# Performance work log

Measured on AMD Instinct MI355X. Metric: run time of the kernel, lower is better.

The kernel has to match this reference:

```python
import jax, jax.numpy as jnp
import numpy as np

DEPTH = 6
N_LEAF = 2 ** DEPTH          # 64
GATE_COUNT = N_LEAF - 1      # 63
IN_F = 512
OUT_F = 512
BATCH = 1024


def setup_inputs() -> dict:
    key = jax.random.key(0)
    k1, k2, k3 = jax.random.split(key, 3)
    x = jax.random.normal(k1, (BATCH, IN_F), dtype=jnp.float32)
    gw = jax.random.normal(k2, (IN_F, GATE_COUNT), dtype=jnp.float32)
    gb = jnp.zeros((GATE_COUNT,), dtype=jnp.float32)
    pw = jax.random.normal(k3, (OUT_F, IN_F, N_LEAF), dtype=jnp.float32)
    pb = jnp.zeros((OUT_F, N_LEAF), dtype=jnp.float32)
    return {"x": x, "gw": gw, "gb": gb, "pw": pw, "pb": pb}


def _leaf_probs(x, gw, gb, depth):
    # gatings: sigmoid(x @ gw + gb), shape [B, gate_count]
    g = jax.nn.sigmoid(x @ gw + gb)
    B = x.shape[0]
    dens = jnp.ones((B, 1), dtype=x.dtype)  # root density
    offset = 0
    for d in range(depth):
        n = 2 ** d
        gp = g[:, offset:offset + n]                    # parent gatings [B, n]
        # left child multiplies by g, right child by (1 - g), interleaved
        pair = jnp.stack([gp, 1.0 - gp], axis=-1).reshape(B, 2 * n)
        dens = jnp.repeat(dens, 2, axis=1) * pair        # [B, 2n]
        offset += n
    return dens  # [B, n_leaf]


def reference(x, gw, gb, pw, pb):
    leaf = _leaf_probs(x, gw, gb, DEPTH)                 # [B, L]
    # per-leaf linear projections, then mix with leaf probabilities
    y = jnp.einsum('bi,oil->bol', x, pw)                 # [B, O, L]
    out = jnp.einsum('bol,bl->bo', y, leaf) + leaf @ pb.T
    return out
```

## Files before the change

kernel.cpp:

```cpp
#include <hip/hip_runtime.h>
#include <hip/hip_bf16.h>

#define TDEPTH 6
#define NLEAF 64
#define NGATE 63
#define INF 512
#define OUTF 512
#define BATCH 1024

#define BM 128
#define BN 32
#define SPLITK 16
#define THREADS 128
#define NPL 32

typedef __attribute__((ext_vector_type(4)))  float f32x4;
typedef __attribute__((ext_vector_type(16))) float f32x16;
typedef __attribute__((ext_vector_type(8)))  __bf16 bf16x8;

__device__ __forceinline__ bf16x8 pack8(f32x4 a, f32x4 b) {
  bf16x8 w;
  w[0] = (__bf16)a[0]; w[1] = (__bf16)a[1];
  w[2] = (__bf16)a[2]; w[3] = (__bf16)a[3];
  w[4] = (__bf16)b[0]; w[5] = (__bf16)b[1];
  w[6] = (__bf16)b[2]; w[7] = (__bf16)b[3];
  return w;
}

__global__ __launch_bounds__(256) void prep_kernel(
    const float* __restrict__ x, const float* __restrict__ gw,
    const float* __restrict__ gb, const float* __restrict__ pw,
    const float* __restrict__ pb, float* __restrict__ leaf,
    __bf16* __restrict__ pwb) {
  const int tid = threadIdx.x;
  if (blockIdx.x < 256) {
    const int wid = tid >> 6, lane = tid & 63;
    const int b = blockIdx.x * 4 + wid;
    __shared__ float g[4][NLEAF];
    if (lane < NGATE) {
      const float* xr = x + (size_t)b * INF;
      float a0 = 0.f, a1 = 0.f, a2 = 0.f, a3 = 0.f;
      #pragma unroll 4
      for (int i = 0; i < INF; i += 4) {
        a0 += xr[i + 0] * gw[(i + 0) * NGATE + lane];
        a1 += xr[i + 1] * gw[(i + 1) * NGATE + lane];
        a2 += xr[i + 2] * gw[(i + 2) * NGATE + lane];
        a3 += xr[i + 3] * gw[(i + 3) * NGATE + lane];
      }
      float t = (a0 + a1) + (a2 + a3) + gb[lane];
      g[wid][lane] = 1.0f / (1.0f + __expf(-t));
    }
    __syncthreads();
    float p = 1.0f;
    #pragma unroll
    for (int d = 0; d < TDEPTH; d++) {
      int prefix = lane >> (TDEPTH - 1 - d);
      int node = (1 << d) - 1 + (prefix >> 1);
      float gv = g[wid][node];
      p *= (prefix & 1) ? (1.0f - gv) : gv;
    }
    leaf[(size_t)b * NLEAF + lane] = p;
  } else {
    const unsigned Q = (blockIdx.x - 256) * 256 + tid;
    const unsigned tile = Q >> 8;
    const unsigned nb32 = tile / 513;
    const unsigned i = tile - nb32 * 513;
    const unsigned q = Q & 255;
    const unsigned r = q >> 3;
    const unsigned g = (q & 7) ^ (r & 7);
    const unsigned o = nb32 * 32 + r;
    const float* src = (i < INF) ? (pw + ((size_t)o * INF + i) * NLEAF + g * 8)
                                 : (pb + (size_t)o * NLEAF + g * 8);
    f32x4 a = *(const f32x4*)src, b = *(const f32x4*)(src + 4);
    *(bf16x8*)((char*)pwb + (size_t)Q * 16) = pack8(a, b);
  }
}

__device__ __forceinline__ void gload_lds16(const void* g, void* l) {
  __builtin_amdgcn_global_load_lds(
      (const __attribute__((address_space(1))) void*)g,
      (__attribute__((address_space(3))) void*)l, 16, 0, 0);
}

__global__ __launch_bounds__(THREADS, 4) void gemm_kernel(
    const __bf16* __restrict__ pwb, const float* __restrict__ x,
    const float* __restrict__ leaf, float* __restrict__ partial) {
  __shared__ __align__(16) __bf16 Bsm[3][2048];
  __shared__ __align__(16) __bf16 xsm[NPL][BM];

  const int tid = threadIdx.x, lane = tid & 63, w = tid >> 6;
  const int lo = lane & 31, half = lane >> 5;

  const int L = ((int)blockIdx.x & 7) * 256 + ((int)blockIdx.x >> 3);
  const int mb = L & 7;
  const int rest = L >> 3;
  const int nb = rest & 15, s = rest >> 4;
  const int m0 = mb * BM, o0 = nb * BN;
  const int cs = s * NPL;
  const int count = NPL + (s == SPLITK - 1 ? 1 : 0);

  bf16x8 lfb[2][4];
  #pragma unroll
  for (int mt = 0; mt < 2; mt++) {
    const float* lr =
        leaf + (size_t)(m0 + w * 64 + mt * 32 + lo) * NLEAF + half * 8;
    #pragma unroll
    for (int t4 = 0; t4 < 4; t4++)
      lfb[mt][t4] = pack8(*(const f32x4*)(lr + t4 * 16),
                          *(const f32x4*)(lr + t4 * 16 + 4));
  }

  {
    const float* src = x + (size_t)(m0 + tid) * INF + cs;
    #pragma unroll
    for (int c4 = 0; c4 < NPL / 4; c4++) {
      f32x4 v = *(const f32x4*)(src + c4 * 4);
      #pragma unroll
      for (int j = 0; j < 4; j++) xsm[c4 * 4 + j][tid] = (__bf16)v[j];
    }
  }

  const char* tb = (const char*)pwb + ((size_t)(nb * 513 + cs) << 12);

  auto stage = [&](char* dstb, int t) {
    const char* srcb = tb + ((size_t)t << 12);
    #pragma unroll
    for (int rnd = 0; rnd < 2; rnd++)
      gload_lds16(srcb + rnd * 2048 + tid * 16, dstb + rnd * 2048 + w * 1024);
  };

  f32x16 acc0 = (f32x16)(0.f), acc1 = (f32x16)(0.f);
  const unsigned swz = (unsigned)(lo & 7) << 4;

  auto do_step = [&](const char* bufc, int t) {
    float xv0 = 1.0f, xv1 = 1.0f;
    if (t < NPL) {
      xv0 = (float)xsm[t][w * 64 + lo];
      xv1 = (float)xsm[t][w * 64 + 32 + lo];
    }
    bf16x8 af[4];
    #pragma unroll
    for (int t4 = 0; t4 < 4; t4++)
      af[t4] = *(const bf16x8*)(bufc + lo * 128 +
                                (((unsigned)(t4 * 32 + half * 16)) ^ swz));
    {
      f32x16 D = (f32x16)(0.f);
      #pragma unroll
      for (int t4 = 0; t4 < 4; t4++)
        D = __builtin_amdgcn_mfma_f32_32x32x16_bf16(af[t4], lfb[0][t4], D, 0, 0, 0);
      acc0 += D * xv0;
    }
    {
      f32x16 D = (f32x16)(0.f);
      #pragma unroll
      for (int t4 = 0; t4 < 4; t4++)
        D = __builtin_amdgcn_mfma_f32_32x32x16_bf16(af[t4], lfb[1][t4], D, 0, 0, 0);
      acc1 += D * xv1;
    }
  };

  char* bA = (char*)&Bsm[0][0];
  char* bB = (char*)&Bsm[1][0];
  char* bC = (char*)&Bsm[2][0];

  stage(bA, 0);
  stage(bB, 1);
  __builtin_amdgcn_sched_barrier(0);
  asm volatile("s_waitcnt vmcnt(2) lgkmcnt(0)" ::: "memory");
  __builtin_amdgcn_s_barrier();
  __builtin_amdgcn_sched_barrier(0);

  for (int t = 0; t < count - 2; ++t) {
    stage(bC, t + 2);
    do_step(bA, t);
    __builtin_amdgcn_sched_barrier(0);
    asm volatile("s_waitcnt vmcnt(2) lgkmcnt(0)" ::: "memory");
    __builtin_amdgcn_s_barrier();
    __builtin_amdgcn_sched_barrier(0);
    char* tmp = bA; bA = bB; bB = bC; bC = tmp;
  }
  do_step(bA, count - 2);
  __builtin_amdgcn_sched_barrier(0);
  asm volatile("s_waitcnt vmcnt(0) lgkmcnt(0)" ::: "memory");
  __builtin_amdgcn_s_barrier();
  __builtin_amdgcn_sched_barrier(0);
  do_step(bB, count - 1);

  #pragma unroll
  for (int mt = 0; mt < 2; mt++) {
    float* dstb = partial + ((size_t)s * OUTF + o0) * BATCH +
                  (m0 + w * 64 + mt * 32);
    const f32x16 a = mt ? acc1 : acc0;
    #pragma unroll
    for (int e = 0; e < 16; e++) {
      int row = (e & 3) + 8 * (e >> 2) + 4 * half;
      dstb[(size_t)row * BATCH + lo] = a[e];
    }
  }
}

__global__ __launch_bounds__(256) void reduce_kernel(
    const float* __restrict__ partial, float* __restrict__ out) {
  __shared__ float tile[32][65];
  const int t = threadIdx.x;
  const int O0 = ((int)blockIdx.x >> 4) * 32;
  const int B0 = ((int)blockIdx.x & 15) * 64;
  #pragma unroll
  for (int rep = 0; rep < 8; rep++) {
    const int idx = rep * 256 + t;
    const int o = idx >> 6, b = idx & 63;
    float sum = 0.f;
    #pragma unroll
    for (int s = 0; s < SPLITK; s++)
      sum += partial[((size_t)s * OUTF + O0 + o) * BATCH + B0 + b];
    tile[o][b] = sum;
  }
  __syncthreads();
  #pragma unroll
  for (int rep = 0; rep < 8; rep++) {
    const int idx = rep * 256 + t;
    const int b = idx >> 5, o = idx & 31;
    out[(size_t)(B0 + b) * OUTF + O0 + o] = tile[o][b];
  }
}

extern "C" void kernel_launch(void* const* d_in, const int* in_sizes, int n_in,
                              void* d_out, int out_size, void* d_ws, size_t ws_size,
                              hipStream_t stream) {
  const float* x  = (const float*)d_in[0];
  const float* gw = (const float*)d_in[1];
  const float* gb = (const float*)d_in[2];
  const float* pw = (const float*)d_in[3];
  const float* pb = (const float*)d_in[4];
  float* out = (float*)d_out;

  float*  leaf    = (float*)d_ws;
  __bf16* pwb     = (__bf16*)((char*)d_ws + (256 << 10));
  float*  partial = (float*)((char*)d_ws + (256 << 10) + (size_t)16 * 513 * 4096);

  prep_kernel<<<256 + 8208, 256, 0, stream>>>(x, gw, gb, pw, pb, leaf, pwb);
  gemm_kernel<<<8 * 16 * SPLITK, THREADS, 0, stream>>>(pwb, x, leaf, partial);
  reduce_kernel<<<256, 256, 0, stream>>>(partial, out);
}
```

Before: 75.68 us.

## Retile gemm to single-wave blocks with fp16 and scaled-operand MFMA chaining

Moves the GEMM from bf16 to fp16. It switches to 64-thread single-wavefront blocks that each handle 64 batch rows by 32 output features over a split-K of 8. The x scaling is folded into the leaf operand with packed half multiplies, so the MFMAs accumulate directly instead of using a temporary plus a vector FMA. The block barriers go away because each wave now owns its LDS buffers, and the prep kernel's weight layout and swizzle change to match. The block's B-tile is larger, and folding x into the fp16 leaf values in half precision costs some accuracy and risks overflow or precision loss.

```diff
diff --git a/kernel.cpp b/kernel.cpp
--- a/kernel.cpp
+++ b/kernel.cpp
@@ -7,23 +7,19 @@
 #define INF 512
 #define OUTF 512
 #define BATCH 1024
-
-#define BM 128
-#define BN 32
-#define SPLITK 16
-#define THREADS 128
-#define NPL 32
-
+#define SPLITK 8
+#define NPL 64
+
+typedef _Float16 f16;
+typedef __attribute__((ext_vector_type(2)))  f16 f16x2;
+typedef __attribute__((ext_vector_type(8)))  f16 f16x8;
 typedef __attribute__((ext_vector_type(4)))  float f32x4;
 typedef __attribute__((ext_vector_type(16))) float f32x16;
-typedef __attribute__((ext_vector_type(8)))  __bf16 bf16x8;
-
-__device__ __forceinline__ bf16x8 pack8(f32x4 a, f32x4 b) {
-  bf16x8 w;
-  w[0] = (__bf16)a[0]; w[1] = (__bf16)a[1];
-  w[2] = (__bf16)a[2]; w[3] = (__bf16)a[3];
-  w[4] = (__bf16)b[0]; w[5] = (__bf16)b[1];
-  w[6] = (__bf16)b[2]; w[7] = (__bf16)b[3];
+
+__device__ __forceinline__ f16x8 pack8h(f32x4 a, f32x4 b) {
+  f16x8 w;
+  w[0] = (f16)a[0]; w[1] = (f16)a[1]; w[2] = (f16)a[2]; w[3] = (f16)a[3];
+  w[4] = (f16)b[0]; w[5] = (f16)b[1]; w[6] = (f16)b[2]; w[7] = (f16)b[3];
   return w;
 }
 
@@ -31,7 +27,7 @@
     const float* __restrict__ x, const float* __restrict__ gw,
     const float* __restrict__ gb, const float* __restrict__ pw,
     const float* __restrict__ pb, float* __restrict__ leaf,
-    __bf16* __restrict__ pwb) {
+    f16* __restrict__ pwh) {
   const int tid = threadIdx.x;
   if (blockIdx.x < 256) {
     const int wid = tid >> 6, lane = tid & 63;
@@ -60,20 +56,21 @@
       p *= (prefix & 1) ? (1.0f - gv) : gv;
     }
     leaf[(size_t)b * NLEAF + lane] = p;
-  } else {
-    const unsigned Q = (blockIdx.x - 256) * 256 + tid;
-    const unsigned tile = Q >> 8;
-    const unsigned nb32 = tile / 513;
-    const unsigned i = tile - nb32 * 513;
-    const unsigned q = Q & 255;
-    const unsigned r = q >> 3;
-    const unsigned g = (q & 7) ^ (r & 7);
-    const unsigned o = nb32 * 32 + r;
-    const float* src = (i < INF) ? (pw + ((size_t)o * INF + i) * NLEAF + g * 8)
-                                 : (pb + (size_t)o * NLEAF + g * 8);
-    f32x4 a = *(const f32x4*)src, b = *(const f32x4*)(src + 4);
-    *(bf16x8*)((char*)pwb + (size_t)Q * 16) = pack8(a, b);
-  }
+    return;
+  }
+  const unsigned Q = (blockIdx.x - 256) * 256 + tid;
+  const unsigned tile = Q >> 8;
+  const unsigned ot = tile / 513;
+  const unsigned i = tile - ot * 513;
+  const unsigned q = Q & 255;
+  const unsigned r = q >> 4, p = q & 15;
+  const unsigned v = p ^ r;
+  const unsigned o = ot * 32 + r + 16 * (v >> 3);
+  const unsigned kg = v & 7;
+  const float* src = (i < INF) ? (pw + ((size_t)o * INF + i) * NLEAF + kg * 8)
+                               : (pb + (size_t)o * NLEAF + kg * 8);
+  f32x4 a = *(const f32x4*)src, b = *(const f32x4*)(src + 4);
+  *(f16x8*)((char*)pwh + (size_t)Q * 16) = pack8h(a, b);
 }
 
 __device__ __forceinline__ void gload_lds16(const void* g, void* l) {
@@ -82,80 +79,82 @@
       (__attribute__((address_space(3))) void*)l, 16, 0, 0);
 }
 
-__global__ __launch_bounds__(THREADS, 4) void gemm_kernel(
-    const __bf16* __restrict__ pwb, const float* __restrict__ x,
+__global__ __launch_bounds__(64, 2) void gemm_kernel(
+    const f16* __restrict__ pwh, const float* __restrict__ x,
     const float* __restrict__ leaf, float* __restrict__ partial) {
-  __shared__ __align__(16) __bf16 Bsm[3][2048];
-  __shared__ __align__(16) __bf16 xsm[NPL][BM];
-
-  const int tid = threadIdx.x, lane = tid & 63, w = tid >> 6;
+  __shared__ __align__(16) char Bsm[3][4096];
+  __shared__ unsigned short xsm[NPL][64];
+
+  const int lane = threadIdx.x;
   const int lo = lane & 31, half = lane >> 5;
 
   const int L = ((int)blockIdx.x & 7) * 256 + ((int)blockIdx.x >> 3);
-  const int mb = L & 7;
-  const int rest = L >> 3;
-  const int nb = rest & 15, s = rest >> 4;
-  const int m0 = mb * BM, o0 = nb * BN;
+  const int bt = L & 15;
+  const int p = L >> 4;
+  const int ot = p & 15, s = p >> 4;
+  const int b0 = bt * 64;
   const int cs = s * NPL;
   const int count = NPL + (s == SPLITK - 1 ? 1 : 0);
 
-  bf16x8 lfb[2][4];
+  {
+    const float* xr = x + (size_t)(b0 + lane) * INF + cs;
+    #pragma unroll
+    for (int c4 = 0; c4 < NPL / 4; c4++) {
+      f32x4 v = *(const f32x4*)(xr + c4 * 4);
+      #pragma unroll
+      for (int j = 0; j < 4; j++)
+        xsm[c4 * 4 + j][lane] = __builtin_bit_cast(unsigned short, (f16)v[j]);
+    }
+  }
+
+  f16x8 lfb[2][4];
   #pragma unroll
   for (int mt = 0; mt < 2; mt++) {
-    const float* lr =
-        leaf + (size_t)(m0 + w * 64 + mt * 32 + lo) * NLEAF + half * 8;
+    const float* lr = leaf + (size_t)(b0 + mt * 32 + lo) * NLEAF + half * 8;
     #pragma unroll
     for (int t4 = 0; t4 < 4; t4++)
-      lfb[mt][t4] = pack8(*(const f32x4*)(lr + t4 * 16),
-                          *(const f32x4*)(lr + t4 * 16 + 4));
-  }
-
+      lfb[mt][t4] = pack8h(*(const f32x4*)(lr + t4 * 16),
+                           *(const f32x4*)(lr + t4 * 16 + 4));
+  }
+
+  unsigned rdoff[4];
   {
-    const float* src = x + (size_t)(m0 + tid) * INF + cs;
-    #pragma unroll
-    for (int c4 = 0; c4 < NPL / 4; c4++) {
-      f32x4 v = *(const f32x4*)(src + c4 * 4);
-      #pragma unroll
-      for (int j = 0; j < 4; j++) xsm[c4 * 4 + j][tid] = (__bf16)v[j];
-    }
-  }
-
-  const char* tb = (const char*)pwb + ((size_t)(nb * 513 + cs) << 12);
-
+    const unsigned r = (unsigned)(lo & 15);
+    const unsigned hb = ((unsigned)(lo >> 4)) * 128 + (unsigned)half * 16;
+    #pragma unroll
+    for (int t4 = 0; t4 < 4; t4++)
+      rdoff[t4] = r * 256 + ((hb + t4 * 32) ^ (r << 4));
+  }
+
+  const char* tb = (const char*)pwh + ((size_t)(ot * 513 + cs) << 12) +
+                   (size_t)lane * 16;
   auto stage = [&](char* dstb, int t) {
     const char* srcb = tb + ((size_t)t << 12);
     #pragma unroll
-    for (int rnd = 0; rnd < 2; rnd++)
-      gload_lds16(srcb + rnd * 2048 + tid * 16, dstb + rnd * 2048 + w * 1024);
+    for (int j = 0; j < 4; j++)
+      gload_lds16(srcb + j * 1024, dstb + j * 1024);
   };
 
   f32x16 acc0 = (f32x16)(0.f), acc1 = (f32x16)(0.f);
-  const unsigned swz = (unsigned)(lo & 7) << 4;
 
   auto do_step = [&](const char* bufc, int t) {
-    float xv0 = 1.0f, xv1 = 1.0f;
+    unsigned pr0 = 0x3C003C00u, pr1 = 0x3C003C00u;
     if (t < NPL) {
-      xv0 = (float)xsm[t][w * 64 + lo];
-      xv1 = (float)xsm[t][w * 64 + 32 + lo];
-    }
-    bf16x8 af[4];
-    #pragma unroll
-    for (int t4 = 0; t4 < 4; t4++)
-      af[t4] = *(const bf16x8*)(bufc + lo * 128 +
-                                (((unsigned)(t4 * 32 + half * 16)) ^ swz));
-    {
-      f32x16 D = (f32x16)(0.f);
-      #pragma unroll
-      for (int t4 = 0; t4 < 4; t4++)
-        D = __builtin_amdgcn_mfma_f32_32x32x16_bf16(af[t4], lfb[0][t4], D, 0, 0, 0);
-      acc0 += D * xv0;
-    }
-    {
-      f32x16 D = (f32x16)(0.f);
-      #pragma unroll
-      for (int t4 = 0; t4 < 4; t4++)
-        D = __builtin_amdgcn_mfma_f32_32x32x16_bf16(af[t4], lfb[1][t4], D, 0, 0, 0);
-      acc1 += D * xv1;
+      unsigned x0 = xsm[t][lo], x1 = xsm[t][32 + lo];
+      pr0 = x0 | (x0 << 16);
+      pr1 = x1 | (x1 << 16);
+    }
+    f16x2 v0 = __builtin_bit_cast(f16x2, pr0);
+    f16x2 v1 = __builtin_bit_cast(f16x2, pr1);
+    f16x8 xv80 = __builtin_shufflevector(v0, v0, 0, 1, 0, 1, 0, 1, 0, 1);
+    f16x8 xv81 = __builtin_shufflevector(v1, v1, 0, 1, 0, 1, 0, 1, 0, 1);
+    #pragma unroll
+    for (int t4 = 0; t4 < 4; t4++) {
+      f16x8 af = *(const f16x8*)(bufc + rdoff[t4]);
+      f16x8 s0 = lfb[0][t4] * xv80;
+      f16x8 s1 = lfb[1][t4] * xv81;
+      acc0 = __builtin_amdgcn_mfma_f32_32x32x16_f16(af, s0, acc0, 0, 0, 0);
+      acc1 = __builtin_amdgcn_mfma_f32_32x32x16_f16(af, s1, acc1, 0, 0, 0);
     }
   };
 
@@ -165,37 +164,25 @@
 
   stage(bA, 0);
   stage(bB, 1);
-  __builtin_amdgcn_sched_barrier(0);
-  asm volatile("s_waitcnt vmcnt(2) lgkmcnt(0)" ::: "memory");
-  __builtin_amdgcn_s_barrier();
-  __builtin_amdgcn_sched_barrier(0);
+  asm volatile("s_waitcnt lgkmcnt(0)" ::: "memory");
 
   for (int t = 0; t < count - 2; ++t) {
     stage(bC, t + 2);
+    asm volatile("s_waitcnt vmcnt(8)" ::: "memory");
     do_step(bA, t);
-    __builtin_amdgcn_sched_barrier(0);
-    asm volatile("s_waitcnt vmcnt(2) lgkmcnt(0)" ::: "memory");
-    __builtin_amdgcn_s_barrier();
-    __builtin_amdgcn_sched_barrier(0);
     char* tmp = bA; bA = bB; bB = bC; bC = tmp;
   }
+  asm volatile("s_waitcnt vmcnt(4)" ::: "memory");
   do_step(bA, count - 2);
-  __builtin_amdgcn_sched_barrier(0);
-  asm volatile("s_waitcnt vmcnt(0) lgkmcnt(0)" ::: "memory");
-  __builtin_amdgcn_s_barrier();
-  __builtin_amdgcn_sched_barrier(0);
+  asm volatile("s_waitcnt vmcnt(0)" ::: "memory");
   do_step(bB, count - 1);
 
-  #pragma unroll
-  for (int mt = 0; mt < 2; mt++) {
-    float* dstb = partial + ((size_t)s * OUTF + o0) * BATCH +
-                  (m0 + w * 64 + mt * 32);
-    const f32x16 a = mt ? acc1 : acc0;
-    #pragma unroll
-    for (int e = 0; e < 16; e++) {
-      int row = (e & 3) + 8 * (e >> 2) + 4 * half;
-      dstb[(size_t)row * BATCH + lo] = a[e];
-    }
+  float* dstb = partial + ((size_t)s * OUTF + ot * 32) * BATCH + b0;
+  #pragma unroll
+  for (int e = 0; e < 16; e++) {
+    int row = (e & 3) + 8 * (e >> 2) + 4 * half;
+    dstb[(size_t)row * BATCH + lo] = acc0[e];
+    dstb[(size_t)row * BATCH + 32 + lo] = acc1[e];
   }
 }
 
@@ -234,11 +221,11 @@
   const float* pb = (const float*)d_in[4];
   float* out = (float*)d_out;
 
-  float*  leaf    = (float*)d_ws;
-  __bf16* pwb     = (__bf16*)((char*)d_ws + (256 << 10));
-  float*  partial = (float*)((char*)d_ws + (256 << 10) + (size_t)16 * 513 * 4096);
-
-  prep_kernel<<<256 + 8208, 256, 0, stream>>>(x, gw, gb, pw, pb, leaf, pwb);
-  gemm_kernel<<<8 * 16 * SPLITK, THREADS, 0, stream>>>(pwb, x, leaf, partial);
+  float* leaf    = (float*)d_ws;
+  f16*   pwh     = (f16*)((char*)d_ws + (256 << 10));
+  float* partial = (float*)((char*)d_ws + (256 << 10) + (size_t)16 * 513 * 4096);
+
+  prep_kernel<<<256 + 8208, 256, 0, stream>>>(x, gw, gb, pw, pb, leaf, pwh);
+  gemm_kernel<<<2048, 64, 0, stream>>>(pwh, x, leaf, partial);
   reduce_kernel<<<256, 256, 0, stream>>>(partial, out);
 }
```

Result: faster. 72.14 us (-4.7%).
